# Optimization experiments

Hardware: AMD Instinct MI355X
Metric: run time of the kernel (lower is better)

Reference implementation:

```python
import jax, jax.numpy as jnp
import numpy as np

# MACE/molgym-style SimpleModel with max_ell=1, hidden_irreps = 64x0e + 64x1o,
# num_interactions=2, num_elements=10, num_bessel=8, polynomial cutoff p=5, r_max=5.0.
N, E, C, NE, NB, H = 20000, 320000, 64, 10, 8, 64
R_MAX = 5.0
P_CUT = 5


def _mlp(x, W1, W2, W3):
    # radial MLP producing per-edge tensor-product weights (silu nonlinearity)
    h = jax.nn.silu(x @ W1)
    h = jax.nn.silu(h @ W2)
    return h @ W3


def setup_inputs() -> dict:
    key = jax.random.key(0)
    ks = jax.random.split(key, 24)
    positions = jax.random.normal(ks[0], (N, 3), jnp.float32)
    edge_index = jax.random.randint(ks[1], (2, E), 0, N)
    shifts = jnp.zeros((E, 3), jnp.float32)
    species = jax.random.randint(ks[2], (N,), 0, NE)
    node_attrs = jax.nn.one_hot(species, NE, dtype=jnp.float32)

    def w(k, shape, fan_in):
        return jax.random.normal(k, shape, jnp.float32) / np.sqrt(fan_in)

    params = dict(
        W_embed=w(ks[3], (NE, C), NE),
        R1_W1=w(ks[4], (NB, H), NB), R1_W2=w(ks[5], (H, H), H), R1_W3=w(ks[6], (H, 2 * C), H),
        U1_s=w(ks[7], (C, C), C),
        L1_s=w(ks[8], (C, C), C), L1_v=w(ks[9], (C, C), C),
        K1_s=w(ks[10], (C, NE, C), C * NE),
        R2_W1=w(ks[11], (NB, H), NB), R2_W2=w(ks[12], (H, H), H), R2_W3=w(ks[13], (H, 4 * C), H),
        U2_s=w(ks[14], (C, C), C), U2_v=w(ks[15], (C, C), C),
        L2_s=w(ks[16], (2 * C, C), 2 * C), L2_v=w(ks[17], (2 * C, C), 2 * C),
        K2_s=w(ks[18], (C, NE, C), C * NE), K2_v=w(ks[19], (C, NE, C), C * NE),
    )
    return dict(positions=positions, node_attrs=node_attrs, edge_index=edge_index,
                shifts=shifts, **params)


def _forward(positions, node_attrs, shifts, W_embed,
             R1_W1, R1_W2, R1_W3, U1_s, L1_s, L1_v, K1_s,
             R2_W1, R2_W2, R2_W3, U2_s, U2_v, L2_s, L2_v, K2_s, K2_v,
             edge_index):
    snd, rcv = edge_index[0], edge_index[1]
    # edge vectors / lengths
    vec = positions[snd] - positions[rcv] + shifts            # [E,3]
    length = jnp.sqrt(jnp.sum(vec * vec, axis=1, keepdims=True) + 1e-12)  # [E,1]
    unit = vec / length
    # spherical harmonics (normalize=True, component normalization): Y0=1, Y1=sqrt(3)*r_hat
    Y1 = np.float32(np.sqrt(3.0)) * unit                      # [E,3]
    # Bessel radial basis * polynomial cutoff
    n = jnp.arange(1, NB + 1, dtype=jnp.float32)
    bessel = np.float32(np.sqrt(2.0 / R_MAX)) * jnp.sin(n * np.float32(np.pi) * length / R_MAX) / length
    u = length / R_MAX
    p = P_CUT
    poly = (1.0 - 0.5 * (p + 1) * (p + 2) * u ** p
            + p * (p + 2) * u ** (p + 1)
            - 0.5 * p * (p + 1) * u ** (p + 2))
    edge_feats = bessel * (poly * (u < 1.0))                  # [E,NB]
    # node embedding (linear on one-hot species)
    s0 = node_attrs @ W_embed                                 # [N,C]

    # ---- interaction block 1 (input feats: scalars only) ----
    s = s0 @ U1_s                                             # linear_up
    tpw = _mlp(edge_feats, R1_W1, R1_W2, R1_W3).reshape(E, 2, C)
    s_e = s[snd]                                              # gather sender feats
    m_s = tpw[:, 0] * s_e                                     # 0e x 0e -> 0e  [E,C]
    m_v = (tpw[:, 1] * s_e)[:, :, None] * Y1[:, None, :]      # 0e x 1o -> 1o  [E,C,3]
    agg_s = jax.ops.segment_sum(m_s, rcv, num_segments=N)
    agg_v = jax.ops.segment_sum(m_v, rcv, num_segments=N)
    skip_s = jnp.einsum('nu,nv,uvd->nd', s0, node_attrs, K1_s)  # skip tensor product
    s1 = agg_s @ L1_s + skip_s                                # [N,C]
    v1 = jnp.einsum('nci,cd->ndi', agg_v, L1_v)               # [N,C,3]

    # ---- interaction block 2 (input feats: 64x0e + 64x1o) ----
    s = s1 @ U2_s
    v = jnp.einsum('nci,cd->ndi', v1, U2_v)
    tpw = _mlp(edge_feats, R2_W1, R2_W2, R2_W3).reshape(E, 4, C)
    s_e, v_e = s[snd], v[snd]
    mA = tpw[:, 0] * s_e                                      # 0e x 0e -> 0e
    mB = (tpw[:, 1] * s_e)[:, :, None] * Y1[:, None, :]       # 0e x 1o -> 1o
    mC = tpw[:, 2][:, :, None] * v_e                          # 1o x 0e -> 1o
    mD = tpw[:, 3] * (jnp.einsum('eci,ei->ec', v_e, Y1) / np.float32(np.sqrt(3.0)))  # 1o x 1o -> 0e
    mid_s = jnp.concatenate([mA, mD], axis=1)                 # [E,2C]
    mid_v = jnp.concatenate([mB, mC], axis=1)                 # [E,2C,3]
    agg_s = jax.ops.segment_sum(mid_s, rcv, num_segments=N)
    agg_v = jax.ops.segment_sum(mid_v, rcv, num_segments=N)
    skip_s = jnp.einsum('nu,nv,uvd->nd', s1, node_attrs, K2_s)
    skip_v = jnp.einsum('nui,nv,uvd->ndi', v1, node_attrs, K2_v)
    s2 = agg_s @ L2_s + skip_s                                # [N,C]
    v2 = jnp.einsum('nci,cd->ndi', agg_v, L2_v) + skip_v      # [N,C,3]
    return jnp.concatenate([s2, v2.reshape(N, 3 * C)], axis=1)  # [N,4C]


def reference(positions, node_attrs, edge_index, shifts, W_embed,
              R1_W1, R1_W2, R1_W3, U1_s, L1_s, L1_v, K1_s,
              R2_W1, R2_W2, R2_W3, U2_s, U2_v, L2_s, L2_v, K2_s, K2_v):
    return _forward(positions, node_attrs, shifts, W_embed,
                    R1_W1, R1_W2, R1_W3, U1_s, L1_s, L1_v, K1_s,
                    R2_W1, R2_W2, R2_W3, U2_s, U2_v, L2_s, L2_v, K2_s, K2_v,
                    edge_index)
```

## Files before the change

### kernel.cpp

```cpp
#include <hip/hip_runtime.h>

#define NNODES 20000
#define NEDGES 320000
#define NELEM  10
#define NC     (NNODES * 64)

#define OFF_SUP1 ((size_t)0)
#define OFF_AGS1 ((size_t)1 * NC)
#define OFF_AGV1 ((size_t)2 * NC)
#define OFF_AGS2 ((size_t)0)
#define OFF_AGV2 ((size_t)2 * NC)
#define OFF_SUP2 ((size_t)8 * NC)
#define OFF_VUP2 ((size_t)9 * NC)
#define OFF_SKS2 ((size_t)12 * NC)
#define OFF_SKV2 ((size_t)13 * NC)
#define OFF_INT  ((size_t)16 * NC)

typedef __attribute__((ext_vector_type(8))) short bf16x8;
typedef __attribute__((ext_vector_type(4))) float f32x4;

__device__ __forceinline__ float silu(float x) { return x / (1.0f + __expf(-x)); }
__device__ __forceinline__ int rfl(int v) { return __builtin_amdgcn_readfirstlane(v); }
__device__ __forceinline__ int rl_i(int v, int l) { return __builtin_amdgcn_readlane(v, l); }
__device__ __forceinline__ float rl_f(float v, int l) {
    return __int_as_float(__builtin_amdgcn_readlane(__float_as_int(v), l));
}
__device__ __forceinline__ uint2 split2(float x0, float x1) {
    unsigned int b0 = __float_as_uint(x0), b1 = __float_as_uint(x1);
    unsigned int h0 = (b0 + 0x7FFF + ((b0 >> 16) & 1)) & 0xFFFF0000u;
    unsigned int h1 = (b1 + 0x7FFF + ((b1 >> 16) & 1)) & 0xFFFF0000u;
    unsigned int l0 = __float_as_uint(x0 - __uint_as_float(h0));
    unsigned int l1 = __float_as_uint(x1 - __uint_as_float(h1));
    unsigned int hi = (h0 >> 16) | (h1 & 0xFFFF0000u);
    unsigned int lo = ((l0 + 0x7FFF + ((l0 >> 16) & 1)) >> 16)
                    | ((l1 + 0x7FFF + ((l1 >> 16) & 1)) & 0xFFFF0000u);
    return make_uint2(hi, lo);
}

__global__ __launch_bounds__(256) void k_wsplit(
    const float* __restrict__ W3a, const float* __restrict__ W3b,
    unsigned short* __restrict__ out)
{
    int t = blockIdx.x * 256 + threadIdx.x;
    float x; unsigned short *ph, *pl; int idx;
    if (t < 8192) {
        int n = t >> 6, k = t & 63;
        x = W3a[k * 128 + n]; ph = out; pl = out + 8192; idx = n * 64 + k;
    } else {
        int u = t - 8192; int n = u >> 6, k = u & 63;
        x = W3b[k * 256 + n]; ph = out + 16384; pl = out + 32768; idx = n * 64 + k;
    }
    unsigned int b = __float_as_uint(x);
    unsigned int h = (b + 0x7FFF + ((b >> 16) & 1)) & 0xFFFF0000u;
    unsigned int r = __float_as_uint(x - __uint_as_float(h));
    ph[idx] = (unsigned short)(h >> 16);
    pl[idx] = (unsigned short)((r + 0x7FFF + ((r >> 16) & 1)) >> 16);
}

__global__ __launch_bounds__(256) void k_hist(const int* __restrict__ eidx,
                                              int* __restrict__ hist)
{
    int e = blockIdx.x * 256 + threadIdx.x;
    atomicAdd(&hist[eidx[NEDGES + e]], 1);
}

__global__ __launch_bounds__(1024) void k_scan(const int* __restrict__ hist,
                                               int* __restrict__ cursor)
{
    __shared__ int wsum[16];
    __shared__ int gbase;
    int tid = threadIdx.x;
    int lane = tid & 63, wvid = tid >> 6;
    if (tid == 0) gbase = 0;
    __syncthreads();
    for (int seg = 0; seg < 20; ++seg) {
        int i = seg * 1024 + tid;
        int v = (i < NNODES) ? hist[i] : 0;
        int s = v;
        #pragma unroll
        for (int d = 1; d < 64; d <<= 1) {
            int t = __shfl_up(s, d, 64);
            if (lane >= d) s += t;
        }
        if (lane == 63) wsum[wvid] = s;
        __syncthreads();
        if (wvid == 0) {
            int w = (lane < 16) ? wsum[lane] : 0;
            #pragma unroll
            for (int d = 1; d < 16; d <<= 1) {
                int t = __shfl_up(w, d, 64);
                if (lane >= d) w += t;
            }
            if (lane < 16) wsum[lane] = w;
        }
        __syncthreads();
        int wbase = (wvid == 0) ? 0 : wsum[wvid - 1];
        if (i < NNODES) cursor[i] = gbase + wbase + s - v;
        int segtot = wsum[15];
        __syncthreads();
        if (tid == 0) gbase += segtot;
    }
}

__global__ __launch_bounds__(256) void k_scatter(const int* __restrict__ eidx,
                                                 int* __restrict__ cursor,
                                                 int* __restrict__ sorted)
{
    int e = blockIdx.x * 256 + threadIdx.x;
    int pos = atomicAdd(&cursor[eidx[NEDGES + e]], 1);
    sorted[pos] = e;
}

__device__ __forceinline__ void edge_geom(
    int e, const float* __restrict__ pos, const int* __restrict__ eidx,
    const float* __restrict__ shf, int* snd_out, int* rcv_out,
    float feats[8], float y[3])
{
    int snd = eidx[e], rcv = eidx[NEDGES + e];
    *snd_out = snd; *rcv_out = rcv;
    float dx = pos[snd * 3 + 0] - pos[rcv * 3 + 0] + shf[(size_t)e * 3 + 0];
    float dy = pos[snd * 3 + 1] - pos[rcv * 3 + 1] + shf[(size_t)e * 3 + 1];
    float dz = pos[snd * 3 + 2] - pos[rcv * 3 + 2] + shf[(size_t)e * 3 + 2];
    float len = sqrtf(dx * dx + dy * dy + dz * dz + 1e-12f);
    float inv = 1.0f / len;
    float u = len * 0.2f;
    float u2 = u * u, u4 = u2 * u2, u5 = u4 * u, u6 = u5 * u, u7 = u6 * u;
    float cut = (u < 1.0f) ? (1.0f - 21.0f * u5 + 35.0f * u6 - 15.0f * u7) : 0.0f;
    float s = 0.632455532033676f * inv * cut;
    #pragma unroll
    for (int k = 0; k < 8; ++k)
        feats[k] = s * sinf((float)(k + 1) * 0.628318530717959f * len);
    y[0] = 1.73205080756888f * dx * inv;
    y[1] = 1.73205080756888f * dy * inv;
    y[2] = 1.73205080756888f * dz * inv;
}

__global__ __launch_bounds__(256) void k_node_pre(
    const float* __restrict__ attrs, const float* __restrict__ Wemb,
    const float* __restrict__ U1s, float* __restrict__ sUp1)
{
    int lane = threadIdx.x & 63, wv = threadIdx.x >> 6;
    int n = blockIdx.x * 4 + wv;
    __shared__ __align__(16) float s0sh[4][64];
    float s0 = 0.f;
    #pragma unroll
    for (int v = 0; v < NELEM; ++v) s0 += attrs[n * NELEM + v] * Wemb[v * 64 + lane];
    s0sh[wv][lane] = s0;
    __syncthreads();
    float a = 0.f;
    #pragma unroll 8
    for (int k = 0; k < 64; ++k) a += s0sh[wv][k] * U1s[k * 64 + lane];
    sUp1[n * 64 + lane] = a;
}

__global__ __launch_bounds__(256) void k_edge1(
    const float* __restrict__ pos, const int* __restrict__ eidx,
    const float* __restrict__ shf, const int* __restrict__ sorted,
    const float* __restrict__ W1, const float* __restrict__ W2,
    const unsigned short* __restrict__ w3h, const unsigned short* __restrict__ w3l,
    const float* __restrict__ sUp1,
    float* __restrict__ agS1, float* __restrict__ agV1)
{
    const int tid = threadIdx.x;
    const int lane = tid & 63;
    const int mu = rfl(tid >> 6);
    const int e0 = blockIdx.x * 64;
    __shared__ float fsh[64][9];
    __shared__ float ysh[64][3];
    __shared__ int ssh[64], rsh[64];
    __shared__ __align__(16) float h1sh[64][65];
    __shared__ __align__(16) unsigned short h2buf[2][64][72];

    if (tid < 64) {
        int sid = sorted[e0 + tid];
        int snd, rcv; float f[8], y[3];
        edge_geom(sid, pos, eidx, shf, &snd, &rcv, f, y);
        ssh[tid] = snd; rsh[tid] = rcv;
        #pragma unroll
        for (int k = 0; k < 8; ++k) fsh[tid][k] = f[k];
        #pragma unroll
        for (int i = 0; i < 3; ++i) ysh[tid][i] = y[i];
    }
    __syncthreads();

    const int rAll = rsh[lane];
    const int sAll = ssh[lane];
    const float y0A = ysh[lane][0], y1A = ysh[lane][1], y2A = ysh[lane][2];

    {
        float f[8];
        #pragma unroll
        for (int k = 0; k < 8; ++k) f[k] = fsh[lane][k];
        const float* __restrict__ w1b = W1 + mu * 16;
        #pragma unroll
        for (int j = 0; j < 16; ++j) {
            float a = 0.f;
            #pragma unroll
            for (int k = 0; k < 8; ++k) a = fmaf(f[k], w1b[k * 64 + j], a);
            h1sh[lane][mu * 16 + j] = silu(a);
        }
    }
    __syncthreads();

    {
        const float2* __restrict__ w2b = (const float2*)W2 + mu * 8;
        float2 acc[8];
        #pragma unroll
        for (int j = 0; j < 8; ++j) acc[j] = make_float2(0.f, 0.f);
        for (int k = 0; k < 64; ++k) {
            float h = h1sh[lane][k];
            const float2* __restrict__ wk = w2b + k * 32;
            #pragma unroll
            for (int j = 0; j < 8; ++j) {
                float2 w = wk[j];
                acc[j].x = fmaf(h, w.x, acc[j].x);
                acc[j].y = fmaf(h, w.y, acc[j].y);
            }
        }
        #pragma unroll
        for (int j = 0; j < 8; ++j) {
            uint2 p = split2(silu(acc[j].x), silu(acc[j].y));
            *(unsigned int*)&h2buf[0][lane][mu * 16 + 2 * j] = p.x;
            *(unsigned int*)&h2buf[1][lane][mu * 16 + 2 * j] = p.y;
        }
    }
    __syncthreads();

    const int m = mu & 1, hh = mu >> 1;
    const int q = lane >> 4, nl = lane & 15;
    f32x4 accT[4][2];
    for (int mt = 0; mt < 4; ++mt) {
        const unsigned short* ar = &h2buf[0][mt * 16 + nl][0];
        const unsigned short* al = &h2buf[1][mt * 16 + nl][0];
        bf16x8 ah0 = *(const bf16x8*)(ar + q * 8);
        bf16x8 ah1 = *(const bf16x8*)(ar + 32 + q * 8);
        bf16x8 al0 = *(const bf16x8*)(al + q * 8);
        bf16x8 al1 = *(const bf16x8*)(al + 32 + q * 8);
        #pragma unroll
        for (int nt = 0; nt < 2; ++nt) {
            int ng = m * 64 + hh * 32 + nt * 16 + nl;
            const unsigned short* wh = w3h + ng * 64 + q * 8;
            const unsigned short* wl = w3l + ng * 64 + q * 8;
            bf16x8 bh0 = *(const bf16x8*)wh;
            bf16x8 bh1 = *(const bf16x8*)(wh + 32);
            bf16x8 bl0 = *(const bf16x8*)wl;
            bf16x8 bl1 = *(const bf16x8*)(wl + 32);
            f32x4 a = {0.f, 0.f, 0.f, 0.f};
            a = __builtin_amdgcn_mfma_f32_16x16x32_bf16(ah0, bh0, a, 0, 0, 0);
            a = __builtin_amdgcn_mfma_f32_16x16x32_bf16(ah1, bh1, a, 0, 0, 0);
            a = __builtin_amdgcn_mfma_f32_16x16x32_bf16(ah0, bl0, a, 0, 0, 0);
            a = __builtin_amdgcn_mfma_f32_16x16x32_bf16(ah1, bl1, a, 0, 0, 0);
            a = __builtin_amdgcn_mfma_f32_16x16x32_bf16(al0, bh0, a, 0, 0, 0);
            a = __builtin_amdgcn_mfma_f32_16x16x32_bf16(al1, bh1, a, 0, 0, 0);
            accT[mt][nt] = a;
        }
    }
    __syncthreads();

    float (*trS)[64] = (float (*)[64])h1sh;
    float (*trV)[64] = (float (*)[64])&h2buf[0][0][0];
    float (*tr)[64] = (m == 0) ? trS : trV;
    #pragma unroll
    for (int mt = 0; mt < 4; ++mt)
        #pragma unroll
        for (int nt = 0; nt < 2; ++nt)
            #pragma unroll
            for (int r = 0; r < 4; ++r) {
                int e = mt * 16 + q * 4 + r;
                int o = hh * 32 + nt * 16 + nl;
                tr[e][(o + e) & 63] = accT[mt][nt][r];
            }
    __syncthreads();

    float accS = 0.f, a0 = 0.f, a1 = 0.f, a2 = 0.f;
    const int base = hh * 32;
    int cur = rl_i(rAll, base);
    #pragma unroll 8
    for (int i = 0; i < 32; ++i) {
        int e = base + i;
        int rcv = rl_i(rAll, e);
        int snd = rl_i(sAll, e);
        float tv = tr[e][(lane + e) & 63];
        if (rcv != cur) {
            if (m == 0) {
                unsafeAtomicAdd(&agS1[cur * 64 + lane], accS); accS = 0.f;
            } else {
                unsafeAtomicAdd(&agV1[cur * 192 +       lane], a0);
                unsafeAtomicAdd(&agV1[cur * 192 +  64 + lane], a1);
                unsafeAtomicAdd(&agV1[cur * 192 + 128 + lane], a2);
                a0 = a1 = a2 = 0.f;
            }
            cur = rcv;
        }
        float msg = tv * sUp1[snd * 64 + lane];
        if (m == 0) {
            accS += msg;
        } else {
            a0 += msg * rl_f(y0A, e);
            a1 += msg * rl_f(y1A, e);
            a2 += msg * rl_f(y2A, e);
        }
    }
    if (m == 0) {
        unsafeAtomicAdd(&agS1[cur * 64 + lane], accS);
    } else {
        unsafeAtomicAdd(&agV1[cur * 192 +       lane], a0);
        unsafeAtomicAdd(&agV1[cur * 192 +  64 + lane], a1);
        unsafeAtomicAdd(&agV1[cur * 192 + 128 + lane], a2);
    }
}

__global__ __launch_bounds__(256) void k_node_mid(
    const float* __restrict__ attrs, const float* __restrict__ Wemb,
    const float* __restrict__ K1s, const float* __restrict__ L1s,
    const float* __restrict__ L1v,
    const float* __restrict__ U2s, const float* __restrict__ U2v,
    const float* __restrict__ K2s, const float* __restrict__ K2v,
    const float* __restrict__ agS1, const float* __restrict__ agV1,
    float* __restrict__ sUp2, float* __restrict__ vUp2,
    float* __restrict__ skS2, float* __restrict__ skV2)
{
    int lane = threadIdx.x & 63, wv = threadIdx.x >> 6;
    int n = blockIdx.x * 4 + wv;
    __shared__ float aSsh[4][64];
    __shared__ float aVsh[4][3][64];
    __shared__ float s0sh[4][64];
    __shared__ float s1sh[4][64];
    __shared__ float v1sh[4][3][64];

    int sp = 0;
    #pragma unroll
    for (int v = 0; v < NELEM; ++v) if (attrs[n * NELEM + v] > 0.5f) sp = v;
    aSsh[wv][lane] = agS1[n * 64 + lane];
    #pragma unroll
    for (int i = 0; i < 3; ++i) aVsh[wv][i][lane] = agV1[n * 192 + i * 64 + lane];
    s0sh[wv][lane] = Wemb[sp * 64 + lane];
    __syncthreads();

    float s1 = 0.f;
    #pragma unroll 8
    for (int k = 0; k < 64; ++k) s1 += aSsh[wv][k] * L1s[k * 64 + lane];
    #pragma unroll 8
    for (int k = 0; k < 64; ++k) s1 += s0sh[wv][k] * K1s[(k * NELEM + sp) * 64 + lane];
    float v1[3] = {0.f, 0.f, 0.f};
    #pragma unroll 8
    for (int k = 0; k < 64; ++k) {
        float w = L1v[k * 64 + lane];
        v1[0] += aVsh[wv][0][k] * w;
        v1[1] += aVsh[wv][1][k] * w;
        v1[2] += aVsh[wv][2][k] * w;
    }
    s1sh[wv][lane] = s1;
    #pragma unroll
    for (int i = 0; i < 3; ++i) v1sh[wv][i][lane] = v1[i];
    __syncthreads();

    float su = 0.f, ks = 0.f;
    float vu[3] = {0.f, 0.f, 0.f}, kv[3] = {0.f, 0.f, 0.f};
    #pragma unroll 8
    for (int k = 0; k < 64; ++k) su += s1sh[wv][k] * U2s[k * 64 + lane];
    #pragma unroll 8
    for (int k = 0; k < 64; ++k) ks += s1sh[wv][k] * K2s[(k * NELEM + sp) * 64 + lane];
    #pragma unroll 8
    for (int k = 0; k < 64; ++k) {
        float w = U2v[k * 64 + lane];
        vu[0] += v1sh[wv][0][k] * w;
        vu[1] += v1sh[wv][1][k] * w;
        vu[2] += v1sh[wv][2][k] * w;
    }
    #pragma unroll 8
    for (int k = 0; k < 64; ++k) {
        float w = K2v[(k * NELEM + sp) * 64 + lane];
        kv[0] += v1sh[wv][0][k] * w;
        kv[1] += v1sh[wv][1][k] * w;
        kv[2] += v1sh[wv][2][k] * w;
    }
    sUp2[n * 64 + lane] = su;
    skS2[n * 64 + lane] = ks;
    #pragma unroll
    for (int i = 0; i < 3; ++i) {
        vUp2[n * 192 + i * 64 + lane] = vu[i];
        skV2[n * 192 + i * 64 + lane] = kv[i];
    }
}

__global__ __launch_bounds__(256) void k_edge2(
    const float* __restrict__ pos, const int* __restrict__ eidx,
    const float* __restrict__ shf, const int* __restrict__ sorted,
    const float* __restrict__ W1, const float* __restrict__ W2,
    const unsigned short* __restrict__ w3h, const unsigned short* __restrict__ w3l,
    const float* __restrict__ sUp2, const float* __restrict__ vUp2,
    float* __restrict__ agS2, float* __restrict__ agV2)
{
    const int tid = threadIdx.x;
    const int lane = tid & 63;
    const int mu = rfl(tid >> 6);
    const int e0 = blockIdx.x * 64;
    __shared__ float fsh[64][9];
    __shared__ float ysh[64][3];
    __shared__ int ssh[64], rsh[64];
    __shared__ __align__(16) float h1sh[64][65];
    __shared__ __align__(16) unsigned short h2buf[2][64][72];

    if (tid < 64) {
        int sid = sorted[e0 + tid];
        int snd, rcv; float f[8], y[3];
        edge_geom(sid, pos, eidx, shf, &snd, &rcv, f, y);
        ssh[tid] = snd; rsh[tid] = rcv;
        #pragma unroll
        for (int k = 0; k < 8; ++k) fsh[tid][k] = f[k];
        #pragma unroll
        for (int i = 0; i < 3; ++i) ysh[tid][i] = y[i];
    }
    __syncthreads();

    const int rAll = rsh[lane];
    const int sAll = ssh[lane];
    const float y0A = ysh[lane][0], y1A = ysh[lane][1], y2A = ysh[lane][2];

    {
        float f[8];
        #pragma unroll
        for (int k = 0; k < 8; ++k) f[k] = fsh[lane][k];
        const float* __restrict__ w1b = W1 + mu * 16;
        #pragma unroll
        for (int j = 0; j < 16; ++j) {
            float a = 0.f;
            #pragma unroll
            for (int k = 0; k < 8; ++k) a = fmaf(f[k], w1b[k * 64 + j], a);
            h1sh[lane][mu * 16 + j] = silu(a);
        }
    }
    __syncthreads();

    {
        const float2* __restrict__ w2b = (const float2*)W2 + mu * 8;
        float2 acc[8];
        #pragma unroll
        for (int j = 0; j < 8; ++j) acc[j] = make_float2(0.f, 0.f);
        for (int k = 0; k < 64; ++k) {
            float h = h1sh[lane][k];
            const float2* __restrict__ wk = w2b + k * 32;
            #pragma unroll
            for (int j = 0; j < 8; ++j) {
                float2 w = wk[j];
                acc[j].x = fmaf(h, w.x, acc[j].x);
                acc[j].y = fmaf(h, w.y, acc[j].y);
            }
        }
        #pragma unroll
        for (int j = 0; j < 8; ++j) {
            uint2 p = split2(silu(acc[j].x), silu(acc[j].y));
            *(unsigned int*)&h2buf[0][lane][mu * 16 + 2 * j] = p.x;
            *(unsigned int*)&h2buf[1][lane][mu * 16 + 2 * j] = p.y;
        }
    }
    __syncthreads();

    const int q = lane >> 4, nl = lane & 15;
    float (*tr)[64] = (float (*)[64])((float*)h1sh + (size_t)mu * 1024);
    float accS = 0.f, a0 = 0.f, a1 = 0.f, a2 = 0.f;
    int cur = rl_i(rAll, 0);
    for (int mt = 0; mt < 4; ++mt) {
        const unsigned short* ar = &h2buf[0][mt * 16 + nl][0];
        const unsigned short* al = &h2buf[1][mt * 16 + nl][0];
        bf16x8 ah0 = *(const bf16x8*)(ar + q * 8);
        bf16x8 ah1 = *(const bf16x8*)(ar + 32 + q * 8);
        bf16x8 al0 = *(const bf16x8*)(al + q * 8);
        bf16x8 al1 = *(const bf16x8*)(al + 32 + q * 8);
        #pragma unroll
        for (int nt = 0; nt < 4; ++nt) {
            int ng = mu * 64 + nt * 16 + nl;
            const unsigned short* wh = w3h + ng * 64 + q * 8;
            const unsigned short* wl = w3l + ng * 64 + q * 8;
            bf16x8 bh0 = *(const bf16x8*)wh;
            bf16x8 bh1 = *(const bf16x8*)(wh + 32);
            bf16x8 bl0 = *(const bf16x8*)wl;
            bf16x8 bl1 = *(const bf16x8*)(wl + 32);
            f32x4 a = {0.f, 0.f, 0.f, 0.f};
            a = __builtin_amdgcn_mfma_f32_16x16x32_bf16(ah0, bh0, a, 0, 0, 0);
            a = __builtin_amdgcn_mfma_f32_16x16x32_bf16(ah1, bh1, a, 0, 0, 0);
            a = __builtin_amdgcn_mfma_f32_16x16x32_bf16(ah0, bl0, a, 0, 0, 0);
            a = __builtin_amdgcn_mfma_f32_16x16x32_bf16(ah1, bl1, a, 0, 0, 0);
            a = __builtin_amdgcn_mfma_f32_16x16x32_bf16(al0, bh0, a, 0, 0, 0);
            a = __builtin_amdgcn_mfma_f32_16x16x32_bf16(al1, bh1, a, 0, 0, 0);
            #pragma unroll
            for (int r = 0; r < 4; ++r) {
                int li = q * 4 + r;
                tr[li][(nt * 16 + nl + li) & 63] = a[r];
            }
        }
        #pragma unroll 4
        for (int i = 0; i < 16; ++i) {
            int e = mt * 16 + i;
            int rcv = rl_i(rAll, e);
            int snd = rl_i(sAll, e);
            float tv = tr[i][(lane + i) & 63];
            if (rcv != cur) {
                if (mu == 0) {
                    unsafeAtomicAdd(&agS2[cur * 128 + lane], accS); accS = 0.f;
                } else if (mu == 1) {
                    unsafeAtomicAdd(&agV2[cur * 384 + 0 * 128 + lane], a0);
                    unsafeAtomicAdd(&agV2[cur * 384 + 1 * 128 + lane], a1);
                    unsafeAtomicAdd(&agV2[cur * 384 + 2 * 128 + lane], a2);
                    a0 = a1 = a2 = 0.f;
                } else if (mu == 2) {
                    unsafeAtomicAdd(&agV2[cur * 384 + 0 * 128 + 64 + lane], a0);
                    unsafeAtomicAdd(&agV2[cur * 384 + 1 * 128 + 64 + lane], a1);
                    unsafeAtomicAdd(&agV2[cur * 384 + 2 * 128 + 64 + lane], a2);
                    a0 = a1 = a2 = 0.f;
                } else {
                    unsafeAtomicAdd(&agS2[cur * 128 + 64 + lane], accS); accS = 0.f;
                }
                cur = rcv;
            }
            if (mu == 0) {
                accS += tv * sUp2[snd * 64 + lane];
            } else if (mu == 1) {
                float msg = tv * sUp2[snd * 64 + lane];
                a0 += msg * rl_f(y0A, e);
                a1 += msg * rl_f(y1A, e);
                a2 += msg * rl_f(y2A, e);
            } else if (mu == 2) {
                a0 += tv * vUp2[snd * 192 +       lane];
                a1 += tv * vUp2[snd * 192 +  64 + lane];
                a2 += tv * vUp2[snd * 192 + 128 + lane];
            } else {
                float v0 = vUp2[snd * 192 +       lane];
                float v1 = vUp2[snd * 192 +  64 + lane];
                float v2 = vUp2[snd * 192 + 128 + lane];
                accS += tv * (v0 * rl_f(y0A, e) + v1 * rl_f(y1A, e)
                            + v2 * rl_f(y2A, e)) * 0.577350269189626f;
            }
        }
    }
    if (mu == 0) {
        unsafeAtomicAdd(&agS2[cur * 128 + lane], accS);
    } else if (mu == 1) {
        unsafeAtomicAdd(&agV2[cur * 384 + 0 * 128 + lane], a0);
        unsafeAtomicAdd(&agV2[cur * 384 + 1 * 128 + lane], a1);
        unsafeAtomicAdd(&agV2[cur * 384 + 2 * 128 + lane], a2);
    } else if (mu == 2) {
        unsafeAtomicAdd(&agV2[cur * 384 + 0 * 128 + 64 + lane], a0);
        unsafeAtomicAdd(&agV2[cur * 384 + 1 * 128 + 64 + lane], a1);
        unsafeAtomicAdd(&agV2[cur * 384 + 2 * 128 + 64 + lane], a2);
    } else {
        unsafeAtomicAdd(&agS2[cur * 128 + 64 + lane], accS);
    }
}

__global__ __launch_bounds__(256) void k_node_out(
    const float* __restrict__ L2s, const float* __restrict__ L2v,
    const float* __restrict__ agS2, const float* __restrict__ agV2,
    const float* __restrict__ skS2, const float* __restrict__ skV2,
    float* __restrict__ out)
{
    int lane = threadIdx.x & 63, wv = threadIdx.x >> 6;
    int n = blockIdx.x * 4 + wv;
    __shared__ __align__(16) float aS[4][128];
    __shared__ __align__(16) float aV[4][3][128];

    aS[wv][lane]      = agS2[n * 128 + lane];
    aS[wv][64 + lane] = agS2[n * 128 + 64 + lane];
    #pragma unroll
    for (int i = 0; i < 3; ++i) {
        aV[wv][i][lane]      = agV2[n * 384 + i * 128 + lane];
        aV[wv][i][64 + lane] = agV2[n * 384 + i * 128 + 64 + lane];
    }
    __syncthreads();

    float s2 = skS2[n * 64 + lane];
    #pragma unroll 8
    for (int u = 0; u < 128; ++u) s2 += aS[wv][u] * L2s[u * 64 + lane];
    float v2[3];
    #pragma unroll
    for (int i = 0; i < 3; ++i) v2[i] = skV2[n * 192 + i * 64 + lane];
    #pragma unroll 8
    for (int u = 0; u < 128; ++u) {
        float w = L2v[u * 64 + lane];
        v2[0] += aV[wv][0][u] * w;
        v2[1] += aV[wv][1][u] * w;
        v2[2] += aV[wv][2][u] * w;
    }
    out[(size_t)n * 256 + lane] = s2;
    #pragma unroll
    for (int i = 0; i < 3; ++i)
        out[(size_t)n * 256 + 64 + lane * 3 + i] = v2[i];
}

extern "C" void kernel_launch(void* const* d_in, const int* in_sizes, int n_in,
                              void* d_out, int out_size, void* d_ws, size_t ws_size,
                              hipStream_t stream)
{
    (void)in_sizes; (void)n_in; (void)out_size; (void)ws_size;
    const float* positions  = (const float*)d_in[0];
    const float* node_attrs = (const float*)d_in[1];
    const int*   edge_index = (const int*)d_in[2];
    const float* shifts     = (const float*)d_in[3];
    const float* W_embed    = (const float*)d_in[4];
    const float* R1W1 = (const float*)d_in[5];
    const float* R1W2 = (const float*)d_in[6];
    const float* R1W3 = (const float*)d_in[7];
    const float* U1s  = (const float*)d_in[8];
    const float* L1s  = (const float*)d_in[9];
    const float* L1v  = (const float*)d_in[10];
    const float* K1s  = (const float*)d_in[11];
    const float* R2W1 = (const float*)d_in[12];
    const float* R2W2 = (const float*)d_in[13];
    const float* R2W3 = (const float*)d_in[14];
    const float* U2s  = (const float*)d_in[15];
    const float* U2v  = (const float*)d_in[16];
    const float* L2s  = (const float*)d_in[17];
    const float* L2v  = (const float*)d_in[18];
    const float* K2s  = (const float*)d_in[19];
    const float* K2v  = (const float*)d_in[20];

    float* wsf = (float*)d_ws;
    int*   wsi = (int*)(wsf + OFF_INT);
    int* hist   = wsi;
    int* cursor = wsi + 20000;
    int* sorted = wsi + 40000;
    unsigned short* wsh = (unsigned short*)(wsi + 360000);
    const unsigned short* w3a_hi = wsh;
    const unsigned short* w3a_lo = wsh + 8192;
    const unsigned short* w3b_hi = wsh + 16384;
    const unsigned short* w3b_lo = wsh + 32768;

    hipMemsetAsync(wsf + OFF_AGS1, 0, (size_t)4 * NC * sizeof(float), stream);
    hipMemsetAsync(hist, 0, 20000 * sizeof(int), stream);

    k_wsplit<<<96, 256, 0, stream>>>(R1W3, R2W3, wsh);
    k_hist<<<NEDGES / 256, 256, 0, stream>>>(edge_index, hist);
    k_scan<<<1, 1024, 0, stream>>>(hist, cursor);
    k_scatter<<<NEDGES / 256, 256, 0, stream>>>(edge_index, cursor, sorted);

    k_node_pre<<<NNODES / 4, 256, 0, stream>>>(node_attrs, W_embed, U1s, wsf + OFF_SUP1);
    k_edge1<<<NEDGES / 64, 256, 0, stream>>>(positions, edge_index, shifts, sorted,
                                             R1W1, R1W2, w3a_hi, w3a_lo,
                                             wsf + OFF_SUP1, wsf + OFF_AGS1, wsf + OFF_AGV1);
    k_node_mid<<<NNODES / 4, 256, 0, stream>>>(node_attrs, W_embed, K1s, L1s, L1v,
                                               U2s, U2v, K2s, K2v,
                                               wsf + OFF_AGS1, wsf + OFF_AGV1,
                                               wsf + OFF_SUP2, wsf + OFF_VUP2,
                                               wsf + OFF_SKS2, wsf + OFF_SKV2);
    hipMemsetAsync(wsf + OFF_AGS2, 0, (size_t)8 * NC * sizeof(float), stream);
    k_edge2<<<NEDGES / 64, 256, 0, stream>>>(positions, edge_index, shifts, sorted,
                                             R2W1, R2W2, w3b_hi, w3b_lo,
                                             wsf + OFF_SUP2, wsf + OFF_VUP2,
                                             wsf + OFF_AGS2, wsf + OFF_AGV2);
    k_node_out<<<NNODES / 4, 256, 0, stream>>>(L2s, L2v, wsf + OFF_AGS2, wsf + OFF_AGV2,
                                               wsf + OFF_SKS2, wsf + OFF_SKV2,
                                               (float*)d_out);
}
```

Baseline: 724.4 us.

## Repartition edge kernels so each wave owns 16 edges across all channels

Both edge kernels now give each wave 16 edges and all output-weight columns. Previously each wave owned a slice of the weight columns for all 64 edges. Edge geometry is spread over all 256 threads instead of 64, sender features are prefetched into registers before the MFMA stage, and a single shared-memory pool is reused. This is meant to remove the per-wave branch divergence on path type, cut sender-feature reloads and shorten the serial geometry step. In exchange, each wave issues atomics for every path, and register pressure rises under the launch bound of three blocks.

```diff
diff --git a/kernel.cpp b/kernel.cpp
--- a/kernel.cpp
+++ b/kernel.cpp
@@ -16,6 +16,8 @@
 #define OFF_SKV2 ((size_t)13 * NC)
 #define OFF_INT  ((size_t)16 * NC)
 
+#define SMEM_BYTES 52480
+
 typedef __attribute__((ext_vector_type(8))) short bf16x8;
 typedef __attribute__((ext_vector_type(4))) float f32x4;
 
@@ -111,30 +113,6 @@
     sorted[pos] = e;
 }
 
-__device__ __forceinline__ void edge_geom(
-    int e, const float* __restrict__ pos, const int* __restrict__ eidx,
-    const float* __restrict__ shf, int* snd_out, int* rcv_out,
-    float feats[8], float y[3])
-{
-    int snd = eidx[e], rcv = eidx[NEDGES + e];
-    *snd_out = snd; *rcv_out = rcv;
-    float dx = pos[snd * 3 + 0] - pos[rcv * 3 + 0] + shf[(size_t)e * 3 + 0];
-    float dy = pos[snd * 3 + 1] - pos[rcv * 3 + 1] + shf[(size_t)e * 3 + 1];
-    float dz = pos[snd * 3 + 2] - pos[rcv * 3 + 2] + shf[(size_t)e * 3 + 2];
-    float len = sqrtf(dx * dx + dy * dy + dz * dz + 1e-12f);
-    float inv = 1.0f / len;
-    float u = len * 0.2f;
-    float u2 = u * u, u4 = u2 * u2, u5 = u4 * u, u6 = u5 * u, u7 = u6 * u;
-    float cut = (u < 1.0f) ? (1.0f - 21.0f * u5 + 35.0f * u6 - 15.0f * u7) : 0.0f;
-    float s = 0.632455532033676f * inv * cut;
-    #pragma unroll
-    for (int k = 0; k < 8; ++k)
-        feats[k] = s * sinf((float)(k + 1) * 0.628318530717959f * len);
-    y[0] = 1.73205080756888f * dx * inv;
-    y[1] = 1.73205080756888f * dy * inv;
-    y[2] = 1.73205080756888f * dz * inv;
-}
-
 __global__ __launch_bounds__(256) void k_node_pre(
     const float* __restrict__ attrs, const float* __restrict__ Wemb,
     const float* __restrict__ U1s, float* __restrict__ sUp1)
@@ -153,7 +131,7 @@
     sUp1[n * 64 + lane] = a;
 }
 
-__global__ __launch_bounds__(256) void k_edge1(
+__global__ __launch_bounds__(256, 3) void k_edge1(
     const float* __restrict__ pos, const int* __restrict__ eidx,
     const float* __restrict__ shf, const int* __restrict__ sorted,
     const float* __restrict__ W1, const float* __restrict__ W2,
@@ -161,25 +139,43 @@
     const float* __restrict__ sUp1,
     float* __restrict__ agS1, float* __restrict__ agV1)
 {
+    __shared__ __align__(16) char smem[SMEM_BYTES];
+    float (*ysh)[3]   = (float (*)[3])(smem);
+    int*  ssh         = (int*)(smem + 768);
+    int*  rsh         = (int*)(smem + 1024);
+    float (*h1sh)[65] = (float (*)[65])(smem + 1280);
+    float (*fsh)[9]   = (float (*)[9])(smem + 17920);
+    unsigned short (*h2buf)[64][72] = (unsigned short (*)[64][72])(smem + 34048);
+
     const int tid = threadIdx.x;
     const int lane = tid & 63;
-    const int mu = rfl(tid >> 6);
+    const int w = rfl(tid >> 6);
     const int e0 = blockIdx.x * 64;
-    __shared__ float fsh[64][9];
-    __shared__ float ysh[64][3];
-    __shared__ int ssh[64], rsh[64];
-    __shared__ __align__(16) float h1sh[64][65];
-    __shared__ __align__(16) unsigned short h2buf[2][64][72];
-
-    if (tid < 64) {
-        int sid = sorted[e0 + tid];
-        int snd, rcv; float f[8], y[3];
-        edge_geom(sid, pos, eidx, shf, &snd, &rcv, f, y);
-        ssh[tid] = snd; rsh[tid] = rcv;
-        #pragma unroll
-        for (int k = 0; k < 8; ++k) fsh[tid][k] = f[k];
-        #pragma unroll
-        for (int i = 0; i < 3; ++i) ysh[tid][i] = y[i];
+
+    {
+        int e = tid >> 2, sub = tid & 3;
+        int sid = sorted[e0 + e];
+        int snd = eidx[sid], rcv = eidx[NEDGES + sid];
+        float dx = pos[snd * 3 + 0] - pos[rcv * 3 + 0] + shf[(size_t)sid * 3 + 0];
+        float dy = pos[snd * 3 + 1] - pos[rcv * 3 + 1] + shf[(size_t)sid * 3 + 1];
+        float dz = pos[snd * 3 + 2] - pos[rcv * 3 + 2] + shf[(size_t)sid * 3 + 2];
+        float len = sqrtf(dx * dx + dy * dy + dz * dz + 1e-12f);
+        float inv = 1.0f / len;
+        float u = len * 0.2f;
+        float u2 = u * u, u4 = u2 * u2, u5 = u4 * u, u6 = u5 * u, u7 = u6 * u;
+        float cut = (u < 1.0f) ? (1.0f - 21.0f * u5 + 35.0f * u6 - 15.0f * u7) : 0.0f;
+        float s = 0.632455532033676f * inv * cut;
+        #pragma unroll
+        for (int kk = 0; kk < 2; ++kk) {
+            int k = sub * 2 + kk;
+            fsh[e][k] = s * sinf((float)(k + 1) * 0.628318530717959f * len);
+        }
+        if (sub == 0) {
+            ssh[e] = snd; rsh[e] = rcv;
+            ysh[e][0] = 1.73205080756888f * dx * inv;
+            ysh[e][1] = 1.73205080756888f * dy * inv;
+            ysh[e][2] = 1.73205080756888f * dz * inv;
+        }
     }
     __syncthreads();
 
@@ -191,19 +187,19 @@
         float f[8];
         #pragma unroll
         for (int k = 0; k < 8; ++k) f[k] = fsh[lane][k];
-        const float* __restrict__ w1b = W1 + mu * 16;
+        const float* __restrict__ w1b = W1 + w * 16;
         #pragma unroll
         for (int j = 0; j < 16; ++j) {
             float a = 0.f;
             #pragma unroll
             for (int k = 0; k < 8; ++k) a = fmaf(f[k], w1b[k * 64 + j], a);
-            h1sh[lane][mu * 16 + j] = silu(a);
-        }
-    }
-    __syncthreads();
-
-    {
-        const float2* __restrict__ w2b = (const float2*)W2 + mu * 8;
+            h1sh[lane][w * 16 + j] = silu(a);
+        }
+    }
+    __syncthreads();
+
+    {
+        const float2* __restrict__ w2b = (const float2*)W2 + w * 8;
         float2 acc[8];
         #pragma unroll
         for (int j = 0; j < 8; ++j) acc[j] = make_float2(0.f, 0.f);
@@ -212,102 +208,85 @@
             const float2* __restrict__ wk = w2b + k * 32;
             #pragma unroll
             for (int j = 0; j < 8; ++j) {
-                float2 w = wk[j];
-                acc[j].x = fmaf(h, w.x, acc[j].x);
-                acc[j].y = fmaf(h, w.y, acc[j].y);
+                float2 wv = wk[j];
+                acc[j].x = fmaf(h, wv.x, acc[j].x);
+                acc[j].y = fmaf(h, wv.y, acc[j].y);
             }
         }
         #pragma unroll
         for (int j = 0; j < 8; ++j) {
             uint2 p = split2(silu(acc[j].x), silu(acc[j].y));
-            *(unsigned int*)&h2buf[0][lane][mu * 16 + 2 * j] = p.x;
-            *(unsigned int*)&h2buf[1][lane][mu * 16 + 2 * j] = p.y;
-        }
-    }
-    __syncthreads();
-
-    const int m = mu & 1, hh = mu >> 1;
+            *(unsigned int*)&h2buf[0][lane][w * 16 + 2 * j] = p.x;
+            *(unsigned int*)&h2buf[1][lane][w * 16 + 2 * j] = p.y;
+        }
+    }
+    __syncthreads();
+
     const int q = lane >> 4, nl = lane & 15;
-    f32x4 accT[4][2];
-    for (int mt = 0; mt < 4; ++mt) {
-        const unsigned short* ar = &h2buf[0][mt * 16 + nl][0];
-        const unsigned short* al = &h2buf[1][mt * 16 + nl][0];
-        bf16x8 ah0 = *(const bf16x8*)(ar + q * 8);
-        bf16x8 ah1 = *(const bf16x8*)(ar + 32 + q * 8);
-        bf16x8 al0 = *(const bf16x8*)(al + q * 8);
-        bf16x8 al1 = *(const bf16x8*)(al + 32 + q * 8);
-        #pragma unroll
-        for (int nt = 0; nt < 2; ++nt) {
-            int ng = m * 64 + hh * 32 + nt * 16 + nl;
-            const unsigned short* wh = w3h + ng * 64 + q * 8;
-            const unsigned short* wl = w3l + ng * 64 + q * 8;
-            bf16x8 bh0 = *(const bf16x8*)wh;
-            bf16x8 bh1 = *(const bf16x8*)(wh + 32);
-            bf16x8 bl0 = *(const bf16x8*)wl;
-            bf16x8 bl1 = *(const bf16x8*)(wl + 32);
-            f32x4 a = {0.f, 0.f, 0.f, 0.f};
-            a = __builtin_amdgcn_mfma_f32_16x16x32_bf16(ah0, bh0, a, 0, 0, 0);
-            a = __builtin_amdgcn_mfma_f32_16x16x32_bf16(ah1, bh1, a, 0, 0, 0);
-            a = __builtin_amdgcn_mfma_f32_16x16x32_bf16(ah0, bl0, a, 0, 0, 0);
-            a = __builtin_amdgcn_mfma_f32_16x16x32_bf16(ah1, bl1, a, 0, 0, 0);
-            a = __builtin_amdgcn_mfma_f32_16x16x32_bf16(al0, bh0, a, 0, 0, 0);
-            a = __builtin_amdgcn_mfma_f32_16x16x32_bf16(al1, bh1, a, 0, 0, 0);
-            accT[mt][nt] = a;
-        }
-    }
-    __syncthreads();
-
-    float (*trS)[64] = (float (*)[64])h1sh;
-    float (*trV)[64] = (float (*)[64])&h2buf[0][0][0];
-    float (*tr)[64] = (m == 0) ? trS : trV;
-    #pragma unroll
-    for (int mt = 0; mt < 4; ++mt)
-        #pragma unroll
-        for (int nt = 0; nt < 2; ++nt)
-            #pragma unroll
-            for (int r = 0; r < 4; ++r) {
-                int e = mt * 16 + q * 4 + r;
-                int o = hh * 32 + nt * 16 + nl;
-                tr[e][(o + e) & 63] = accT[mt][nt][r];
-            }
-    __syncthreads();
-
-    float accS = 0.f, a0 = 0.f, a1 = 0.f, a2 = 0.f;
-    const int base = hh * 32;
-    int cur = rl_i(rAll, base);
-    #pragma unroll 8
-    for (int i = 0; i < 32; ++i) {
-        int e = base + i;
+    float* trw = (float*)(smem + 1280) + w * 2048;
+
+    const unsigned short* ar = &h2buf[0][w * 16 + nl][0];
+    const unsigned short* al = &h2buf[1][w * 16 + nl][0];
+    bf16x8 ah0 = *(const bf16x8*)(ar + q * 8);
+    bf16x8 ah1 = *(const bf16x8*)(ar + 32 + q * 8);
+    bf16x8 al0 = *(const bf16x8*)(al + q * 8);
+    bf16x8 al1 = *(const bf16x8*)(al + 32 + q * 8);
+
+    float sreg[16];
+    #pragma unroll
+    for (int i = 0; i < 16; ++i)
+        sreg[i] = sUp1[rl_i(sAll, w * 16 + i) * 64 + lane];
+
+    #pragma unroll
+    for (int nt = 0; nt < 8; ++nt) {
+        int ng = nt * 16 + nl;
+        const unsigned short* wh = w3h + ng * 64 + q * 8;
+        const unsigned short* wl = w3l + ng * 64 + q * 8;
+        bf16x8 bh0 = *(const bf16x8*)wh;
+        bf16x8 bh1 = *(const bf16x8*)(wh + 32);
+        bf16x8 bl0 = *(const bf16x8*)wl;
+        bf16x8 bl1 = *(const bf16x8*)(wl + 32);
+        f32x4 a = {0.f, 0.f, 0.f, 0.f};
+        a = __builtin_amdgcn_mfma_f32_16x16x32_bf16(ah0, bh0, a, 0, 0, 0);
+        a = __builtin_amdgcn_mfma_f32_16x16x32_bf16(ah1, bh1, a, 0, 0, 0);
+        a = __builtin_amdgcn_mfma_f32_16x16x32_bf16(ah0, bl0, a, 0, 0, 0);
+        a = __builtin_amdgcn_mfma_f32_16x16x32_bf16(ah1, bl1, a, 0, 0, 0);
+        a = __builtin_amdgcn_mfma_f32_16x16x32_bf16(al0, bh0, a, 0, 0, 0);
+        a = __builtin_amdgcn_mfma_f32_16x16x32_bf16(al1, bh1, a, 0, 0, 0);
+        #pragma unroll
+        for (int r = 0; r < 4; ++r) {
+            int li = q * 4 + r;
+            trw[li * 128 + ((ng + 4 * li) & 127)] = a[r];
+        }
+    }
+
+    float accS = 0.f, b0 = 0.f, b1 = 0.f, b2 = 0.f;
+    int cur = rl_i(rAll, w * 16);
+    #pragma unroll
+    for (int i = 0; i < 16; ++i) {
+        int e = w * 16 + i;
         int rcv = rl_i(rAll, e);
-        int snd = rl_i(sAll, e);
-        float tv = tr[e][(lane + e) & 63];
         if (rcv != cur) {
-            if (m == 0) {
-                unsafeAtomicAdd(&agS1[cur * 64 + lane], accS); accS = 0.f;
-            } else {
-                unsafeAtomicAdd(&agV1[cur * 192 +       lane], a0);
-                unsafeAtomicAdd(&agV1[cur * 192 +  64 + lane], a1);
-                unsafeAtomicAdd(&agV1[cur * 192 + 128 + lane], a2);
-                a0 = a1 = a2 = 0.f;
-            }
+            unsafeAtomicAdd(&agS1[cur * 64 + lane], accS);
+            unsafeAtomicAdd(&agV1[cur * 192 +       lane], b0);
+            unsafeAtomicAdd(&agV1[cur * 192 +  64 + lane], b1);
+            unsafeAtomicAdd(&agV1[cur * 192 + 128 + lane], b2);
+            accS = b0 = b1 = b2 = 0.f;
             cur = rcv;
         }
-        float msg = tv * sUp1[snd * 64 + lane];
-        if (m == 0) {
-            accS += msg;
-        } else {
-            a0 += msg * rl_f(y0A, e);
-            a1 += msg * rl_f(y1A, e);
-            a2 += msg * rl_f(y2A, e);
-        }
-    }
-    if (m == 0) {
-        unsafeAtomicAdd(&agS1[cur * 64 + lane], accS);
-    } else {
-        unsafeAtomicAdd(&agV1[cur * 192 +       lane], a0);
-        unsafeAtomicAdd(&agV1[cur * 192 +  64 + lane], a1);
-        unsafeAtomicAdd(&agV1[cur * 192 + 128 + lane], a2);
-    }
+        float tv0 = trw[i * 128 + ((lane + 4 * i) & 127)];
+        float tv1 = trw[i * 128 + ((64 + lane + 4 * i) & 127)];
+        float se = sreg[i];
+        accS += tv0 * se;
+        float msg = tv1 * se;
+        b0 += msg * rl_f(y0A, e);
+        b1 += msg * rl_f(y1A, e);
+        b2 += msg * rl_f(y2A, e);
+    }
+    unsafeAtomicAdd(&agS1[cur * 64 + lane], accS);
+    unsafeAtomicAdd(&agV1[cur * 192 +       lane], b0);
+    unsafeAtomicAdd(&agV1[cur * 192 +  64 + lane], b1);
+    unsafeAtomicAdd(&agV1[cur * 192 + 128 + lane], b2);
 }
 
 __global__ __launch_bounds__(256) void k_node_mid(
@@ -384,7 +363,7 @@
     }
 }
 
-__global__ __launch_bounds__(256) void k_edge2(
+__global__ __launch_bounds__(256, 3) void k_edge2(
     const float* __restrict__ pos, const int* __restrict__ eidx,
     const float* __restrict__ shf, const int* __restrict__ sorted,
     const float* __restrict__ W1, const float* __restrict__ W2,
@@ -392,25 +371,43 @@
     const float* __restrict__ sUp2, const float* __restrict__ vUp2,
     float* __restrict__ agS2, float* __restrict__ agV2)
 {
+    __shared__ __align__(16) char smem[SMEM_BYTES];
+    float (*ysh)[3]   = (float (*)[3])(smem);
+    int*  ssh         = (int*)(smem + 768);
+    int*  rsh         = (int*)(smem + 1024);
+    float (*h1sh)[65] = (float (*)[65])(smem + 1280);
+    float (*fsh)[9]   = (float (*)[9])(smem + 17920);
+    unsigned short (*h2buf)[64][72] = (unsigned short (*)[64][72])(smem + 34048);
+
     const int tid = threadIdx.x;
     const int lane = tid & 63;
-    const int mu = rfl(tid >> 6);
+    const int w = rfl(tid >> 6);
     const int e0 = blockIdx.x * 64;
-    __shared__ float fsh[64][9];
-    __shared__ float ysh[64][3];
-    __shared__ int ssh[64], rsh[64];
-    __shared__ __align__(16) float h1sh[64][65];
-    __shared__ __align__(16) unsigned short h2buf[2][64][72];
-
-    if (tid < 64) {
-        int sid = sorted[e0 + tid];
-        int snd, rcv; float f[8], y[3];
-        edge_geom(sid, pos, eidx, shf, &snd, &rcv, f, y);
-        ssh[tid] = snd; rsh[tid] = rcv;
-        #pragma unroll
-        for (int k = 0; k < 8; ++k) fsh[tid][k] = f[k];
-        #pragma unroll
-        for (int i = 0; i < 3; ++i) ysh[tid][i] = y[i];
+
+    {
+        int e = tid >> 2, sub = tid & 3;
+        int sid = sorted[e0 + e];
+        int snd = eidx[sid], rcv = eidx[NEDGES + sid];
+        float dx = pos[snd * 3 + 0] - pos[rcv * 3 + 0] + shf[(size_t)sid * 3 + 0];
+        float dy = pos[snd * 3 + 1] - pos[rcv * 3 + 1] + shf[(size_t)sid * 3 + 1];
+        float dz = pos[snd * 3 + 2] - pos[rcv * 3 + 2] + shf[(size_t)sid * 3 + 2];
+        float len = sqrtf(dx * dx + dy * dy + dz * dz + 1e-12f);
+        float inv = 1.0f / len;
+        float u = len * 0.2f;
+        float u2 = u * u, u4 = u2 * u2, u5 = u4 * u, u6 = u5 * u, u7 = u6 * u;
+        float cut = (u < 1.0f) ? (1.0f - 21.0f * u5 + 35.0f * u6 - 15.0f * u7) : 0.0f;
+        float s = 0.632455532033676f * inv * cut;
+        #pragma unroll
+        for (int kk = 0; kk < 2; ++kk) {
+            int k = sub * 2 + kk;
+            fsh[e][k] = s * sinf((float)(k + 1) * 0.628318530717959f * len);
+        }
+        if (sub == 0) {
+            ssh[e] = snd; rsh[e] = rcv;
+            ysh[e][0] = 1.73205080756888f * dx * inv;
+            ysh[e][1] = 1.73205080756888f * dy * inv;
+            ysh[e][2] = 1.73205080756888f * dz * inv;
+        }
     }
     __syncthreads();
 
@@ -422,19 +419,19 @@
         float f[8];
         #pragma unroll
         for (int k = 0; k < 8; ++k) f[k] = fsh[lane][k];
-        const float* __restrict__ w1b = W1 + mu * 16;
+        const float* __restrict__ w1b = W1 + w * 16;
         #pragma unroll
         for (int j = 0; j < 16; ++j) {
             float a = 0.f;
             #pragma unroll
             for (int k = 0; k < 8; ++k) a = fmaf(f[k], w1b[k * 64 + j], a);
-            h1sh[lane][mu * 16 + j] = silu(a);
-        }
-    }
-    __syncthreads();
-
-    {
-        const float2* __restrict__ w2b = (const float2*)W2 + mu * 8;
+            h1sh[lane][w * 16 + j] = silu(a);
+        }
+    }
+    __syncthreads();
+
+    {
+        const float2* __restrict__ w2b = (const float2*)W2 + w * 8;
         float2 acc[8];
         #pragma unroll
         for (int j = 0; j < 8; ++j) acc[j] = make_float2(0.f, 0.f);
@@ -443,109 +440,149 @@
             const float2* __restrict__ wk = w2b + k * 32;
             #pragma unroll
             for (int j = 0; j < 8; ++j) {
-                float2 w = wk[j];
-                acc[j].x = fmaf(h, w.x, acc[j].x);
-                acc[j].y = fmaf(h, w.y, acc[j].y);
+                float2 wv = wk[j];
+                acc[j].x = fmaf(h, wv.x, acc[j].x);
+                acc[j].y = fmaf(h, wv.y, acc[j].y);
             }
         }
         #pragma unroll
         for (int j = 0; j < 8; ++j) {
             uint2 p = split2(silu(acc[j].x), silu(acc[j].y));
-            *(unsigned int*)&h2buf[0][lane][mu * 16 + 2 * j] = p.x;
-            *(unsigned int*)&h2buf[1][lane][mu * 16 + 2 * j] = p.y;
+            *(unsigned int*)&h2buf[0][lane][w * 16 + 2 * j] = p.x;
+            *(unsigned int*)&h2buf[1][lane][w * 16 + 2 * j] = p.y;
         }
     }
     __syncthreads();
 
     const int q = lane >> 4, nl = lane & 15;
-    float (*tr)[64] = (float (*)[64])((float*)h1sh + (size_t)mu * 1024);
-    float accS = 0.f, a0 = 0.f, a1 = 0.f, a2 = 0.f;
-    int cur = rl_i(rAll, 0);
-    for (int mt = 0; mt < 4; ++mt) {
-        const unsigned short* ar = &h2buf[0][mt * 16 + nl][0];
-        const unsigned short* al = &h2buf[1][mt * 16 + nl][0];
-        bf16x8 ah0 = *(const bf16x8*)(ar + q * 8);
-        bf16x8 ah1 = *(const bf16x8*)(ar + 32 + q * 8);
-        bf16x8 al0 = *(const bf16x8*)(al + q * 8);
-        bf16x8 al1 = *(const bf16x8*)(al + 32 + q * 8);
-        #pragma unroll
-        for (int nt = 0; nt < 4; ++nt) {
-            int ng = mu * 64 + nt * 16 + nl;
-            const unsigned short* wh = w3h + ng * 64 + q * 8;
-            const unsigned short* wl = w3l + ng * 64 + q * 8;
-            bf16x8 bh0 = *(const bf16x8*)wh;
-            bf16x8 bh1 = *(const bf16x8*)(wh + 32);
-            bf16x8 bl0 = *(const bf16x8*)wl;
-            bf16x8 bl1 = *(const bf16x8*)(wl + 32);
-            f32x4 a = {0.f, 0.f, 0.f, 0.f};
-            a = __builtin_amdgcn_mfma_f32_16x16x32_bf16(ah0, bh0, a, 0, 0, 0);
-            a = __builtin_amdgcn_mfma_f32_16x16x32_bf16(ah1, bh1, a, 0, 0, 0);
-            a = __builtin_amdgcn_mfma_f32_16x16x32_bf16(ah0, bl0, a, 0, 0, 0);
-            a = __builtin_amdgcn_mfma_f32_16x16x32_bf16(ah1, bl1, a, 0, 0, 0);
-            a = __builtin_amdgcn_mfma_f32_16x16x32_bf16(al0, bh0, a, 0, 0, 0);
-            a = __builtin_amdgcn_mfma_f32_16x16x32_bf16(al1, bh1, a, 0, 0, 0);
-            #pragma unroll
-            for (int r = 0; r < 4; ++r) {
-                int li = q * 4 + r;
-                tr[li][(nt * 16 + nl + li) & 63] = a[r];
-            }
-        }
-        #pragma unroll 4
+    float* trw = (float*)(smem + 1280) + w * 2048;
+
+    const unsigned short* ar = &h2buf[0][w * 16 + nl][0];
+    const unsigned short* al = &h2buf[1][w * 16 + nl][0];
+    bf16x8 ah0 = *(const bf16x8*)(ar + q * 8);
+    bf16x8 ah1 = *(const bf16x8*)(ar + 32 + q * 8);
+    bf16x8 al0 = *(const bf16x8*)(al + q * 8);
+    bf16x8 al1 = *(const bf16x8*)(al + 32 + q * 8);
+
+    float sreg[16];
+    #pragma unroll
+    for (int i = 0; i < 16; ++i)
+        sreg[i] = sUp2[rl_i(sAll, w * 16 + i) * 64 + lane];
+
+    #pragma unroll
+    for (int nt = 0; nt < 8; ++nt) {
+        int ng = nt * 16 + nl;
+        const unsigned short* wh = w3h + ng * 64 + q * 8;
+        const unsigned short* wl = w3l + ng * 64 + q * 8;
+        bf16x8 bh0 = *(const bf16x8*)wh;
+        bf16x8 bh1 = *(const bf16x8*)(wh + 32);
+        bf16x8 bl0 = *(const bf16x8*)wl;
+        bf16x8 bl1 = *(const bf16x8*)(wl + 32);
+        f32x4 a = {0.f, 0.f, 0.f, 0.f};
+        a = __builtin_amdgcn_mfma_f32_16x16x32_bf16(ah0, bh0, a, 0, 0, 0);
+        a = __builtin_amdgcn_mfma_f32_16x16x32_bf16(ah1, bh1, a, 0, 0, 0);
+        a = __builtin_amdgcn_mfma_f32_16x16x32_bf16(ah0, bl0, a, 0, 0, 0);
+        a = __builtin_amdgcn_mfma_f32_16x16x32_bf16(ah1, bl1, a, 0, 0, 0);
+        a = __builtin_amdgcn_mfma_f32_16x16x32_bf16(al0, bh0, a, 0, 0, 0);
+        a = __builtin_amdgcn_mfma_f32_16x16x32_bf16(al1, bh1, a, 0, 0, 0);
+        #pragma unroll
+        for (int r = 0; r < 4; ++r) {
+            int li = q * 4 + r;
+            trw[li * 128 + ((ng + 4 * li) & 127)] = a[r];
+        }
+    }
+
+    {
+        float accS = 0.f, b0 = 0.f, b1 = 0.f, b2 = 0.f;
+        int cur = rl_i(rAll, w * 16);
+        #pragma unroll
         for (int i = 0; i < 16; ++i) {
-            int e = mt * 16 + i;
+            int e = w * 16 + i;
             int rcv = rl_i(rAll, e);
-            int snd = rl_i(sAll, e);
-            float tv = tr[i][(lane + i) & 63];
             if (rcv != cur) {
-                if (mu == 0) {
-                    unsafeAtomicAdd(&agS2[cur * 128 + lane], accS); accS = 0.f;
-                } else if (mu == 1) {
-                    unsafeAtomicAdd(&agV2[cur * 384 + 0 * 128 + lane], a0);
-                    unsafeAtomicAdd(&agV2[cur * 384 + 1 * 128 + lane], a1);
-                    unsafeAtomicAdd(&agV2[cur * 384 + 2 * 128 + lane], a2);
-                    a0 = a1 = a2 = 0.f;
-                } else if (mu == 2) {
-                    unsafeAtomicAdd(&agV2[cur * 384 + 0 * 128 + 64 + lane], a0);
-                    unsafeAtomicAdd(&agV2[cur * 384 + 1 * 128 + 64 + lane], a1);
-                    unsafeAtomicAdd(&agV2[cur * 384 + 2 * 128 + 64 + lane], a2);
-                    a0 = a1 = a2 = 0.f;
-                } else {
-                    unsafeAtomicAdd(&agS2[cur * 128 + 64 + lane], accS); accS = 0.f;
-                }
+                unsafeAtomicAdd(&agS2[cur * 128 + lane], accS);
+                unsafeAtomicAdd(&agV2[cur * 384 + 0 * 128 + lane], b0);
+                unsafeAtomicAdd(&agV2[cur * 384 + 1 * 128 + lane], b1);
+                unsafeAtomicAdd(&agV2[cur * 384 + 2 * 128 + lane], b2);
+                accS = b0 = b1 = b2 = 0.f;
                 cur = rcv;
             }
-            if (mu == 0) {
-                accS += tv * sUp2[snd * 64 + lane];
-            } else if (mu == 1) {
-                float msg = tv * sUp2[snd * 64 + lane];
-                a0 += msg * rl_f(y0A, e);
-                a1 += msg * rl_f(y1A, e);
-                a2 += msg * rl_f(y2A, e);
-            } else if (mu == 2) {
-                a0 += tv * vUp2[snd * 192 +       lane];
-                a1 += tv * vUp2[snd * 192 +  64 + lane];
-                a2 += tv * vUp2[snd * 192 + 128 + lane];
-            } else {
-                float v0 = vUp2[snd * 192 +       lane];
-                float v1 = vUp2[snd * 192 +  64 + lane];
-                float v2 = vUp2[snd * 192 + 128 + lane];
-                accS += tv * (v0 * rl_f(y0A, e) + v1 * rl_f(y1A, e)
-                            + v2 * rl_f(y2A, e)) * 0.577350269189626f;
+            float tv0 = trw[i * 128 + ((lane + 4 * i) & 127)];
+            float tv1 = trw[i * 128 + ((64 + lane + 4 * i) & 127)];
+            float se = sreg[i];
+            accS += tv0 * se;
+            float msg = tv1 * se;
+            b0 += msg * rl_f(y0A, e);
+            b1 += msg * rl_f(y1A, e);
+            b2 += msg * rl_f(y2A, e);
+        }
+        unsafeAtomicAdd(&agS2[cur * 128 + lane], accS);
+        unsafeAtomicAdd(&agV2[cur * 384 + 0 * 128 + lane], b0);
+        unsafeAtomicAdd(&agV2[cur * 384 + 1 * 128 + lane], b1);
+        unsafeAtomicAdd(&agV2[cur * 384 + 2 * 128 + lane], b2);
+    }
+
+    float vr0[16], vr1[16], vr2[16];
+    #pragma unroll
+    for (int i = 0; i < 16; ++i) {
+        int snd = rl_i(sAll, w * 16 + i);
+        vr0[i] = vUp2[snd * 192 +       lane];
+        vr1[i] = vUp2[snd * 192 +  64 + lane];
+        vr2[i] = vUp2[snd * 192 + 128 + lane];
+    }
+
+    #pragma unroll
+    for (int nt = 0; nt < 8; ++nt) {
+        int c  = nt * 16 + nl;
+        int ng = 128 + c;
+        const unsigned short* wh = w3h + ng * 64 + q * 8;
+        const unsigned short* wl = w3l + ng * 64 + q * 8;
+        bf16x8 bh0 = *(const bf16x8*)wh;
+        bf16x8 bh1 = *(const bf16x8*)(wh + 32);
+        bf16x8 bl0 = *(const bf16x8*)wl;
+        bf16x8 bl1 = *(const bf16x8*)(wl + 32);
+        f32x4 a = {0.f, 0.f, 0.f, 0.f};
+        a = __builtin_amdgcn_mfma_f32_16x16x32_bf16(ah0, bh0, a, 0, 0, 0);
+        a = __builtin_amdgcn_mfma_f32_16x16x32_bf16(ah1, bh1, a, 0, 0, 0);
+        a = __builtin_amdgcn_mfma_f32_16x16x32_bf16(ah0, bl0, a, 0, 0, 0);
+        a = __builtin_amdgcn_mfma_f32_16x16x32_bf16(ah1, bl1, a, 0, 0, 0);
+        a = __builtin_amdgcn_mfma_f32_16x16x32_bf16(al0, bh0, a, 0, 0, 0);
+        a = __builtin_amdgcn_mfma_f32_16x16x32_bf16(al1, bh1, a, 0, 0, 0);
+        #pragma unroll
+        for (int r = 0; r < 4; ++r) {
+            int li = q * 4 + r;
+            trw[li * 128 + ((c + 4 * li) & 127)] = a[r];
+        }
+    }
+
+    {
+        float accD = 0.f, c0 = 0.f, c1 = 0.f, c2 = 0.f;
+        int cur = rl_i(rAll, w * 16);
+        #pragma unroll
+        for (int i = 0; i < 16; ++i) {
+            int e = w * 16 + i;
+            int rcv = rl_i(rAll, e);
+            if (rcv != cur) {
+                unsafeAtomicAdd(&agS2[cur * 128 + 64 + lane], accD);
+                unsafeAtomicAdd(&agV2[cur * 384 + 0 * 128 + 64 + lane], c0);
+                unsafeAtomicAdd(&agV2[cur * 384 + 1 * 128 + 64 + lane], c1);
+                unsafeAtomicAdd(&agV2[cur * 384 + 2 * 128 + 64 + lane], c2);
+                accD = c0 = c1 = c2 = 0.f;
+                cur = rcv;
             }
-        }
-    }
-    if (mu == 0) {
-        unsafeAtomicAdd(&agS2[cur * 128 + lane], accS);
-    } else if (mu == 1) {
-        unsafeAtomicAdd(&agV2[cur * 384 + 0 * 128 + lane], a0);
-        unsafeAtomicAdd(&agV2[cur * 384 + 1 * 128 + lane], a1);
-        unsafeAtomicAdd(&agV2[cur * 384 + 2 * 128 + lane], a2);
-    } else if (mu == 2) {
-        unsafeAtomicAdd(&agV2[cur * 384 + 0 * 128 + 64 + lane], a0);
-        unsafeAtomicAdd(&agV2[cur * 384 + 1 * 128 + 64 + lane], a1);
-        unsafeAtomicAdd(&agV2[cur * 384 + 2 * 128 + 64 + lane], a2);
-    } else {
-        unsafeAtomicAdd(&agS2[cur * 128 + 64 + lane], accS);
+            float tvC = trw[i * 128 + ((lane + 4 * i) & 127)];
+            float tvD = trw[i * 128 + ((64 + lane + 4 * i) & 127)];
+            c0 += tvC * vr0[i];
+            c1 += tvC * vr1[i];
+            c2 += tvC * vr2[i];
+            float dotvy = vr0[i] * rl_f(y0A, e) + vr1[i] * rl_f(y1A, e)
+                        + vr2[i] * rl_f(y2A, e);
+            accD += tvD * dotvy * 0.577350269189626f;
+        }
+        unsafeAtomicAdd(&agS2[cur * 128 + 64 + lane], accD);
+        unsafeAtomicAdd(&agV2[cur * 384 + 0 * 128 + 64 + lane], c0);
+        unsafeAtomicAdd(&agV2[cur * 384 + 1 * 128 + 64 + lane], c1);
+        unsafeAtomicAdd(&agV2[cur * 384 + 2 * 128 + 64 + lane], c2);
     }
 }
 
```

After: 633.1 us. 1.14x faster.
